# Kernel optimization log

Measured on AMD Instinct MI355X. Metric: run time of the kernel, lower is better.

Reference implementation:

```python
import jax, jax.numpy as jnp
import numpy as np

N_NODES = 50000
N_EDGES = 800000
N_GRAPHS = 256
F_IN = 128
H = 64
N_CLASSES = 10


def setup_inputs() -> dict:
    key = jax.random.key(0)
    ks = jax.random.split(key, 12)
    x = jax.random.normal(ks[0], (N_NODES, F_IN), dtype=jnp.float32)
    edge_index = jax.random.randint(ks[1], (2, N_EDGES), 0, N_NODES, dtype=jnp.int64)
    batch = jnp.sort(jax.random.randint(ks[2], (N_NODES,), 0, N_GRAPHS, dtype=jnp.int64))
    def glorot(k, fan_in, fan_out):
        lim = np.sqrt(6.0 / (fan_in + fan_out)).astype(np.float32)
        return jax.random.uniform(k, (fan_in, fan_out), jnp.float32, -lim, lim)
    return {
        "x": x,
        "edge_index": edge_index,
        "batch": batch,
        "W1": glorot(ks[3], F_IN, H), "b1": jnp.zeros((H,), jnp.float32),
        "W2": glorot(ks[4], H, H),    "b2": jnp.zeros((H,), jnp.float32),
        "W3": glorot(ks[5], H, H),    "b3": jnp.zeros((H,), jnp.float32),
        "Wm": glorot(ks[6], H, N_CLASSES), "bm": jnp.zeros((N_CLASSES,), jnp.float32),
    }


def _gcn_norm(edge_index, n_nodes):
    # Add self-loops, unit edge weights, symmetric normalization (PyG gcn_norm).
    loops = jnp.arange(n_nodes, dtype=edge_index.dtype)
    row = jnp.concatenate([edge_index[0], loops])  # source
    col = jnp.concatenate([edge_index[1], loops])  # target (aggregation index)
    deg = jax.ops.segment_sum(jnp.ones_like(col, dtype=jnp.float32), col,
                              num_segments=n_nodes)
    dinv = jnp.where(deg > 0, jax.lax.rsqrt(deg), 0.0)
    norm = dinv[row] * dinv[col]  # [E + N]
    return row, col, norm


def _gcn_conv(x, row, col, norm, W, b, n_nodes):
    h = x @ W                                   # [N, H] dense transform
    msg = h[row] * norm[:, None]                # gather + scale  [E+N, H]
    out = jax.ops.segment_sum(msg, col, num_segments=n_nodes)  # scatter-add
    return out + b


def _l2_normalize(x, eps=1e-12):
    n = jnp.sqrt(jnp.sum(x * x, axis=-1, keepdims=True))
    return x / jnp.maximum(n, eps)


def reference(x, edge_index, batch, W1, b1, W2, b2, W3, b3, Wm, bm):
    n = x.shape[0]
    row, col, norm = _gcn_norm(edge_index, n)
    h = x
    for (W, b) in ((W1, b1), (W2, b2), (W3, b3)):
        h = _gcn_conv(h, row, col, norm, W, b, n)
        h = _l2_normalize(h)       # emb_normalize
        h = jax.nn.relu(h)         # gnn_non_linear
    node_emb = h
    # global_mean_pool over graphs
    sums = jax.ops.segment_sum(h, batch, num_segments=N_GRAPHS)
    counts = jax.ops.segment_sum(jnp.ones((n,), jnp.float32), batch,
                                 num_segments=N_GRAPHS)
    graph_emb = sums / jnp.maximum(counts, 1.0)[:, None]
    logits = graph_emb @ Wm + bm
    probs = jax.nn.softmax(logits, axis=-1)
    return logits, probs, node_emb, graph_emb
```

## Files before the change

### kernel.cpp

```cpp
#include <hip/hip_runtime.h>
#include <math.h>

#define HH 64
#define BSH 8
#define BSZ 256
#define HBLK 256
#define HSTRIDE (HBLK * 256)

typedef _Float16 half_t;
typedef _Float16 half4_t __attribute__((ext_vector_type(4)));

__global__ __launch_bounds__(256, 3)
void k_gemm1_hist(const float* __restrict__ x, const float* __restrict__ W,
                  half_t* __restrict__ out, int n,
                  const int* __restrict__ col, int E, int* __restrict__ ph) {
    constexpr int FIN = 128;
    constexpr int KC = 32;
    __shared__ __align__(16) float Ws[FIN][HH];
    __shared__ __align__(16) float xs_t[KC][68];
    __shared__ int hh[BSZ];
    const int tid = threadIdx.x;
    const int bid = blockIdx.x;

    if (bid < HBLK) {
        hh[tid] = 0;
        __syncthreads();
        for (int e = bid * 256 + tid; e < E; e += HSTRIDE)
            atomicAdd(&hh[col[e] >> BSH], 1);
        __syncthreads();
        ph[bid * BSZ + tid] = hh[tid];
    }

    const int tx = tid & 15;
    const int ty = tid >> 4;
    const int node0 = bid * 64;
    if (node0 >= n) return;

    for (int i = tid * 4; i < FIN * HH; i += 1024)
        *(float4*)&Ws[0][i] = *(const float4*)&W[i];

    float acc[4][4] = {};
    const int rr0 = tid >> 3;
    const int cc  = (tid & 7) * 4;

    for (int kc = 0; kc < FIN; kc += KC) {
        __syncthreads();
        for (int rr = rr0; rr < 64; rr += 32) {
            float4 v = make_float4(0.f, 0.f, 0.f, 0.f);
            if (node0 + rr < n) v = *(const float4*)&x[(size_t)(node0 + rr) * FIN + kc + cc];
            xs_t[cc + 0][rr] = v.x;
            xs_t[cc + 1][rr] = v.y;
            xs_t[cc + 2][rr] = v.z;
            xs_t[cc + 3][rr] = v.w;
        }
        __syncthreads();
#pragma unroll 4
        for (int k = 0; k < KC; ++k) {
            float4 a4 = *(const float4*)&xs_t[k][ty * 4];
            float4 b4 = *(const float4*)&Ws[kc + k][tx * 4];
            acc[0][0] = fmaf(a4.x, b4.x, acc[0][0]);
            acc[0][1] = fmaf(a4.x, b4.y, acc[0][1]);
            acc[0][2] = fmaf(a4.x, b4.z, acc[0][2]);
            acc[0][3] = fmaf(a4.x, b4.w, acc[0][3]);
            acc[1][0] = fmaf(a4.y, b4.x, acc[1][0]);
            acc[1][1] = fmaf(a4.y, b4.y, acc[1][1]);
            acc[1][2] = fmaf(a4.y, b4.z, acc[1][2]);
            acc[1][3] = fmaf(a4.y, b4.w, acc[1][3]);
            acc[2][0] = fmaf(a4.z, b4.x, acc[2][0]);
            acc[2][1] = fmaf(a4.z, b4.y, acc[2][1]);
            acc[2][2] = fmaf(a4.z, b4.z, acc[2][2]);
            acc[2][3] = fmaf(a4.z, b4.w, acc[2][3]);
            acc[3][0] = fmaf(a4.w, b4.x, acc[3][0]);
            acc[3][1] = fmaf(a4.w, b4.y, acc[3][1]);
            acc[3][2] = fmaf(a4.w, b4.z, acc[3][2]);
            acc[3][3] = fmaf(a4.w, b4.w, acc[3][3]);
        }
    }
#pragma unroll
    for (int i = 0; i < 4; ++i) {
        int node = node0 + ty * 4 + i;
        if (node < n) {
            half4_t o = {(half_t)acc[i][0], (half_t)acc[i][1],
                         (half_t)acc[i][2], (half_t)acc[i][3]};
            *(half4_t*)(out + (size_t)node * HH + tx * 4) = o;
        }
    }
}

__global__ __launch_bounds__(256) void k_bscatter2(const int* __restrict__ row,
                                                   const int* __restrict__ col, int E,
                                                   const int* __restrict__ ph,
                                                   int* __restrict__ base,
                                                   int* __restrict__ pair, int nb) {
    __shared__ int cur[BSZ];
    __shared__ int ssc[BSZ];
    const int b = blockIdx.x;
    const int t = threadIdx.x;
    int before = 0, total = 0;
    for (int k = 0; k < HBLK; ++k) {
        int v = ph[k * BSZ + t];
        total += v;
        if (k < b) before += v;
    }
    ssc[t] = total;
    __syncthreads();
    for (int d = 1; d < 256; d <<= 1) {
        int x2 = ssc[t];
        if (t >= d) x2 += ssc[t - d];
        __syncthreads();
        ssc[t] = x2;
        __syncthreads();
    }
    int excl = ssc[t] - total;
    cur[t] = excl + before;
    if (b == 0) {
        if (t < nb) base[t] = excl;
        if (t == 0) base[nb] = E;
    }
    __syncthreads();
    for (int e = b * 256 + t; e < E; e += HSTRIDE) {
        int c = col[e];
        int pos = atomicAdd(&cur[c >> BSH], 1);
        pair[pos] = (row[e] & 0xFFFF) | ((c & (BSZ - 1)) << 16);
    }
}

__global__ __launch_bounds__(256) void k_bcsr(const int* __restrict__ pair,
                                              const int* __restrict__ base,
                                              int* __restrict__ rowptr,
                                              int* __restrict__ cnt,
                                              float* __restrict__ dinv,
                                              int* __restrict__ csr, int n) {
    __shared__ int lcnt[BSZ];
    __shared__ int ssc[BSZ];
    __shared__ int lcur[BSZ];
    const int b = blockIdx.x;
    const int t = threadIdx.x;
    const int nd0 = b << BSH;
    const int e0 = base[b];
    const int e1 = base[b + 1];

    lcnt[t] = 0;
    __syncthreads();
    for (int e = e0 + t; e < e1; e += 256)
        atomicAdd(&lcnt[(pair[e] >> 16) & (BSZ - 1)], 1);
    __syncthreads();
    int v = lcnt[t];
    ssc[t] = v;
    __syncthreads();
    for (int d = 1; d < 256; d <<= 1) {
        int x2 = ssc[t];
        if (t >= d) x2 += ssc[t - d];
        __syncthreads();
        ssc[t] = x2;
        __syncthreads();
    }
    int excl = ssc[t] - v;
    lcur[t] = e0 + excl;
    int node = nd0 + t;
    if (node < n) {
        rowptr[node] = e0 + excl;
        cnt[node]    = v;
        dinv[node]   = rsqrtf((float)(v + 1));
    }
    __syncthreads();
    for (int e = e0 + t; e < e1; e += 256) {
        int pr = pair[e];
        int pos = atomicAdd(&lcur[(pr >> 16) & (BSZ - 1)], 1);
        csr[pos] = pr & 0xFFFF;
    }
}

template<int FIN>
__global__ __launch_bounds__(256, 4)
void k_gemm(const half_t* __restrict__ xin, const float* __restrict__ W,
            const float* __restrict__ dinv, half_t* __restrict__ out, int n) {
    constexpr int KC = 32;
    __shared__ __align__(16) float Ws[FIN][HH];
    __shared__ __align__(16) float xs_t[KC][68];
    const int tid = threadIdx.x;
    const int tx = tid & 15;
    const int ty = tid >> 4;
    const int node0 = blockIdx.x * 64;
    if (node0 >= n) return;

    for (int i = tid * 4; i < FIN * HH; i += 1024)
        *(float4*)&Ws[0][i] = *(const float4*)&W[i];

    float acc[4][4] = {};
    const int rr0 = tid >> 3;
    const int cc  = (tid & 7) * 4;

    for (int kc = 0; kc < FIN; kc += KC) {
        __syncthreads();
        for (int rr = rr0; rr < 64; rr += 32) {
            float4 v = make_float4(0.f, 0.f, 0.f, 0.f);
            if (node0 + rr < n) {
                half4_t hv = *(const half4_t*)(xin + (size_t)(node0 + rr) * FIN + kc + cc);
                v = make_float4((float)hv.x, (float)hv.y, (float)hv.z, (float)hv.w);
            }
            xs_t[cc + 0][rr] = v.x;
            xs_t[cc + 1][rr] = v.y;
            xs_t[cc + 2][rr] = v.z;
            xs_t[cc + 3][rr] = v.w;
        }
        __syncthreads();
#pragma unroll 4
        for (int k = 0; k < KC; ++k) {
            float4 a4 = *(const float4*)&xs_t[k][ty * 4];
            float4 b4 = *(const float4*)&Ws[kc + k][tx * 4];
            acc[0][0] = fmaf(a4.x, b4.x, acc[0][0]);
            acc[0][1] = fmaf(a4.x, b4.y, acc[0][1]);
            acc[0][2] = fmaf(a4.x, b4.z, acc[0][2]);
            acc[0][3] = fmaf(a4.x, b4.w, acc[0][3]);
            acc[1][0] = fmaf(a4.y, b4.x, acc[1][0]);
            acc[1][1] = fmaf(a4.y, b4.y, acc[1][1]);
            acc[1][2] = fmaf(a4.y, b4.z, acc[1][2]);
            acc[1][3] = fmaf(a4.y, b4.w, acc[1][3]);
            acc[2][0] = fmaf(a4.z, b4.x, acc[2][0]);
            acc[2][1] = fmaf(a4.z, b4.y, acc[2][1]);
            acc[2][2] = fmaf(a4.z, b4.z, acc[2][2]);
            acc[2][3] = fmaf(a4.z, b4.w, acc[2][3]);
            acc[3][0] = fmaf(a4.w, b4.x, acc[3][0]);
            acc[3][1] = fmaf(a4.w, b4.y, acc[3][1]);
            acc[3][2] = fmaf(a4.w, b4.z, acc[3][2]);
            acc[3][3] = fmaf(a4.w, b4.w, acc[3][3]);
        }
    }
#pragma unroll
    for (int i = 0; i < 4; ++i) {
        int node = node0 + ty * 4 + i;
        if (node < n) {
            float d = dinv[node];
            half4_t o = {(half_t)(acc[i][0] * d), (half_t)(acc[i][1] * d),
                         (half_t)(acc[i][2] * d), (half_t)(acc[i][3] * d)};
            *(half4_t*)(out + (size_t)node * HH + tx * 4) = o;
        }
    }
}

template<bool WEIGHTED, bool HOUT>
__global__ __launch_bounds__(256) void k_gather_q(const half_t* __restrict__ lin,
                                                  const int* __restrict__ csr,
                                                  const int* __restrict__ rowptr,
                                                  const int* __restrict__ cnt,
                                                  const float* __restrict__ dinv,
                                                  const float* __restrict__ b,
                                                  void* __restrict__ hout, int n) {
    int node = blockIdx.x * 4 + (threadIdx.x >> 6);
    int lane = threadIdx.x & 63;
    if (node >= n) return;
    const int q  = lane >> 4;
    const int fl = (lane & 15) * 4;
    int start = rowptr[node];
    int end = start + cnt[node];
    float di = dinv[node];

    float4 a0 = make_float4(0.f, 0.f, 0.f, 0.f);
    float4 a1 = make_float4(0.f, 0.f, 0.f, 0.f);

    for (int base = start; base < end; base += 64) {
        int m = end - base; if (m > 64) m = 64;
        int idx = base + lane;
        int   sv = (idx < end) ? csr[idx] : 0;
        float wv;
        if (WEIGHTED) wv = (idx < end) ? dinv[sv] : 0.f;
        else          wv = (idx < end) ? 1.f : 0.f;
        for (int j = 0; j < m; j += 16) {
            int l = j + q * 4;
            int   s0 = __shfl(sv, l, 64);
            int   s1 = __shfl(sv, l + 1, 64);
            int   s2 = __shfl(sv, l + 2, 64);
            int   s3 = __shfl(sv, l + 3, 64);
            float w0 = __shfl(wv, l, 64);
            float w1 = __shfl(wv, l + 1, 64);
            float w2 = __shfl(wv, l + 2, 64);
            float w3 = __shfl(wv, l + 3, 64);
            half4_t v0 = *(const half4_t*)&lin[(size_t)s0 * HH + fl];
            half4_t v1 = *(const half4_t*)&lin[(size_t)s1 * HH + fl];
            half4_t v2 = *(const half4_t*)&lin[(size_t)s2 * HH + fl];
            half4_t v3 = *(const half4_t*)&lin[(size_t)s3 * HH + fl];
            a0.x = fmaf(w0, (float)v0.x, a0.x); a0.y = fmaf(w0, (float)v0.y, a0.y);
            a0.z = fmaf(w0, (float)v0.z, a0.z); a0.w = fmaf(w0, (float)v0.w, a0.w);
            a1.x = fmaf(w1, (float)v1.x, a1.x); a1.y = fmaf(w1, (float)v1.y, a1.y);
            a1.z = fmaf(w1, (float)v1.z, a1.z); a1.w = fmaf(w1, (float)v1.w, a1.w);
            a0.x = fmaf(w2, (float)v2.x, a0.x); a0.y = fmaf(w2, (float)v2.y, a0.y);
            a0.z = fmaf(w2, (float)v2.z, a0.z); a0.w = fmaf(w2, (float)v2.w, a0.w);
            a1.x = fmaf(w3, (float)v3.x, a1.x); a1.y = fmaf(w3, (float)v3.y, a1.y);
            a1.z = fmaf(w3, (float)v3.z, a1.z); a1.w = fmaf(w3, (float)v3.w, a1.w);
        }
    }
    float4 acc = make_float4(a0.x + a1.x, a0.y + a1.y, a0.z + a1.z, a0.w + a1.w);
#pragma unroll
    for (int off = 16; off < 64; off <<= 1) {
        acc.x += __shfl_xor(acc.x, off, 64);
        acc.y += __shfl_xor(acc.y, off, 64);
        acc.z += __shfl_xor(acc.z, off, 64);
        acc.w += __shfl_xor(acc.w, off, 64);
    }
    half4_t self = *(const half4_t*)&lin[(size_t)node * HH + fl];
    float sw = WEIGHTED ? di : 1.f;
    acc.x = fmaf(sw, (float)self.x, acc.x);
    acc.y = fmaf(sw, (float)self.y, acc.y);
    acc.z = fmaf(sw, (float)self.z, acc.z);
    acc.w = fmaf(sw, (float)self.w, acc.w);
    float4 b4 = *(const float4*)&b[fl];
    float4 v4 = make_float4(fmaf(di, acc.x, b4.x), fmaf(di, acc.y, b4.y),
                            fmaf(di, acc.z, b4.z), fmaf(di, acc.w, b4.w));
    float ss = v4.x * v4.x + v4.y * v4.y + v4.z * v4.z + v4.w * v4.w;
#pragma unroll
    for (int off = 1; off < 16; off <<= 1) ss += __shfl_xor(ss, off, 64);
    float inv = 1.f / fmaxf(sqrtf(ss), 1e-12f);
    v4.x = fmaxf(v4.x * inv, 0.f);
    v4.y = fmaxf(v4.y * inv, 0.f);
    v4.z = fmaxf(v4.z * inv, 0.f);
    v4.w = fmaxf(v4.w * inv, 0.f);
    if (q == 0) {
        if constexpr (HOUT) {
            half4_t o = {(half_t)v4.x, (half_t)v4.y, (half_t)v4.z, (half_t)v4.w};
            *(half4_t*)((half_t*)hout + (size_t)node * HH + fl) = o;
        } else {
            *(float4*)((float*)hout + (size_t)node * HH + fl) = v4;
        }
    }
}

__global__ __launch_bounds__(256) void k_poolfinal(const float* __restrict__ node_emb,
                                                   const int* __restrict__ batch,
                                                   const float* __restrict__ Wm,
                                                   const float* __restrict__ bm,
                                                   float* __restrict__ logits,
                                                   float* __restrict__ probs,
                                                   float* __restrict__ graph_emb, int n) {
    __shared__ float part[4][HH];
    __shared__ float semb[HH];
    __shared__ float slog[16];
    const int g = blockIdx.x;
    const int tid = threadIdx.x;
    const int lane = tid & 63, w = tid >> 6;

    int lo = 0, hi = n;
    while (lo < hi) { int mid = (lo + hi) >> 1; if (batch[mid] < g) lo = mid + 1; else hi = mid; }
    const int s = lo;
    hi = n;
    while (lo < hi) { int mid = (lo + hi) >> 1; if (batch[mid] < g + 1) lo = mid + 1; else hi = mid; }
    const int e2 = lo;

    float acc = 0.f;
    for (int i = s + w; i < e2; i += 4) acc += node_emb[(size_t)i * HH + lane];
    part[w][lane] = acc;
    __syncthreads();
    if (tid < HH) {
        float m = part[0][tid] + part[1][tid] + part[2][tid] + part[3][tid];
        m /= fmaxf((float)(e2 - s), 1.f);
        graph_emb[(size_t)g * HH + tid] = m;
        semb[tid] = m;
    }
    __syncthreads();
    if (tid < 10) {
        float a2 = bm[tid];
        for (int k = 0; k < HH; ++k) a2 = fmaf(semb[k], Wm[k * 10 + tid], a2);
        slog[tid] = a2;
    }
    __syncthreads();
    if (tid < 10) {
        float mx = -1e30f;
        for (int j = 0; j < 10; ++j) mx = fmaxf(mx, slog[j]);
        float den = 0.f;
        for (int j = 0; j < 10; ++j) den += __expf(slog[j] - mx);
        float lg = slog[tid];
        logits[g * 10 + tid] = lg;
        probs[g * 10 + tid] = __expf(lg - mx) / den;
    }
}


extern "C" void kernel_launch(void* const* d_in, const int* in_sizes, int n_in,
                              void* d_out, int out_size, void* d_ws, size_t ws_size,
                              hipStream_t stream) {
    const float* x     = (const float*)d_in[0];
    const int*   ei    = (const int*)  d_in[1];
    const int*   batch = (const int*)  d_in[2];
    const float* W1 = (const float*)d_in[3];  const float* b1 = (const float*)d_in[4];
    const float* W2 = (const float*)d_in[5];  const float* b2 = (const float*)d_in[6];
    const float* W3 = (const float*)d_in[7];  const float* b3 = (const float*)d_in[8];
    const float* Wm = (const float*)d_in[9];  const float* bm = (const float*)d_in[10];

    const int N = in_sizes[2];
    const int E = in_sizes[1] / 2;
    const int G = (out_size - N * HH) / (2 * 10 + HH);
    const int NB = (N + BSZ - 1) >> BSH;

    const int* row = ei;
    const int* col = ei + E;

    float* out       = (float*)d_out;
    float* logits    = out;
    float* probs     = out + (size_t)G * 10;
    float* node_emb  = out + (size_t)2 * G * 10;
    float* graph_emb = node_emb + (size_t)N * HH;

    char* w = (char*)d_ws;
    auto alloc = [&](size_t bytes) { char* p = w; w += (bytes + 255) & ~(size_t)255; return p; };
    float* dinv    = (float*)alloc((size_t)N * 4);
    int*   cnt     = (int*)  alloc((size_t)N * 4);
    int*   rowptr  = (int*)  alloc((size_t)N * 4);
    int*   ph      = (int*)  alloc((size_t)HBLK * BSZ * 4);
    int*   base    = (int*)  alloc((size_t)(NB + 1) * 4);
    int*   pairbuf = (int*)  alloc((size_t)E * 4);
    int*   csr     = (int*)  alloc((size_t)E * 4);
    half_t* bufA   = (half_t*)alloc((size_t)N * HH * 2);
    half_t* bufB   = (half_t*)alloc((size_t)N * HH * 2);

    const int B = 256;
    dim3 blk(B);
    int node_blocks = (N + 3) / 4;
    int gemm_blocks = (N + 63) / 64;
    int g1_blocks = gemm_blocks > HBLK ? gemm_blocks : HBLK;

    k_gemm1_hist<<<g1_blocks, blk, 0, stream>>>(x, W1, bufA, N, col, E, ph);
    k_bscatter2<<<HBLK, blk, 0, stream>>>(row, col, E, ph, base, pairbuf, NB);
    k_bcsr<<<NB, blk, 0, stream>>>(pairbuf, base, rowptr, cnt, dinv, csr, N);

    k_gather_q<true, true><<<node_blocks, blk, 0, stream>>>(bufA, csr, rowptr, cnt, dinv, b1, bufB, N);
    k_gemm<64><<<gemm_blocks, blk, 0, stream>>>(bufB, W2, dinv, bufA, N);
    k_gather_q<false, true><<<node_blocks, blk, 0, stream>>>(bufA, csr, rowptr, cnt, dinv, b2, bufB, N);
    k_gemm<64><<<gemm_blocks, blk, 0, stream>>>(bufB, W3, dinv, bufA, N);
    k_gather_q<false, false><<<node_blocks, blk, 0, stream>>>(bufA, csr, rowptr, cnt, dinv, b3, node_emb, N);

    k_poolfinal<<<G, blk, 0, stream>>>(node_emb, batch, Wm, bm, logits, probs, graph_emb, N);
}
```

Measured before the change: 269.9 us.

## Split features into two half-planes and defer L2 normalisation to consumers

Node feature buffers are split into two 32-wide fp16 planes. Each gather kernel launches twice as many blocks, one per plane, so the randomly gathered working set per pass is halved and should sit better in cache. The gather now writes unnormalised pre-activation values plus per-plane sums of squares; the following GEMM and the pooling kernel apply the L2 normalisation and ReLU while loading. This adds per-row norm reads and doubles the index and CSR traffic in the gather, and the pool kernel now also writes node_emb.

```diff
diff --git a/kernel.cpp b/kernel.cpp
--- a/kernel.cpp
+++ b/kernel.cpp
@@ -2,17 +2,19 @@
 #include <math.h>
 
 #define HH 64
+#define HF 32
 #define BSH 8
 #define BSZ 256
 #define HBLK 256
 #define HSTRIDE (HBLK * 256)
 
 typedef _Float16 half_t;
+typedef _Float16 half2_t __attribute__((ext_vector_type(2)));
 typedef _Float16 half4_t __attribute__((ext_vector_type(4)));
 
 __global__ __launch_bounds__(256, 3)
 void k_gemm1_hist(const float* __restrict__ x, const float* __restrict__ W,
-                  half_t* __restrict__ out, int n,
+                  half_t* __restrict__ lo, half_t* __restrict__ hi, int n,
                   const int* __restrict__ col, int E, int* __restrict__ ph) {
     constexpr int FIN = 128;
     constexpr int KC = 32;
@@ -82,7 +84,8 @@
         if (node < n) {
             half4_t o = {(half_t)acc[i][0], (half_t)acc[i][1],
                          (half_t)acc[i][2], (half_t)acc[i][3]};
-            *(half4_t*)(out + (size_t)node * HH + tx * 4) = o;
+            if (tx < 8) *(half4_t*)&lo[(size_t)node * HF + tx * 4]        = o;
+            else        *(half4_t*)&hi[(size_t)node * HF + tx * 4 - 32]   = o;
         }
     }
 }
@@ -173,8 +176,10 @@
 
 template<int FIN>
 __global__ __launch_bounds__(256, 4)
-void k_gemm(const half_t* __restrict__ xin, const float* __restrict__ W,
-            const float* __restrict__ dinv, half_t* __restrict__ out, int n) {
+void k_gemm(const half_t* __restrict__ xlo, const half_t* __restrict__ xhi,
+            const float* __restrict__ ssLo, const float* __restrict__ ssHi,
+            const float* __restrict__ W, const float* __restrict__ dinv,
+            half_t* __restrict__ olo, half_t* __restrict__ ohi, int n) {
     constexpr int KC = 32;
     __shared__ __align__(16) float Ws[FIN][HH];
     __shared__ __align__(16) float xs_t[KC][68];
@@ -194,10 +199,17 @@
     for (int kc = 0; kc < FIN; kc += KC) {
         __syncthreads();
         for (int rr = rr0; rr < 64; rr += 32) {
+            int r = node0 + rr;
             float4 v = make_float4(0.f, 0.f, 0.f, 0.f);
-            if (node0 + rr < n) {
-                half4_t hv = *(const half4_t*)(xin + (size_t)(node0 + rr) * FIN + kc + cc);
-                v = make_float4((float)hv.x, (float)hv.y, (float)hv.z, (float)hv.w);
+            if (r < n) {
+                float invr = 1.f / fmaxf(sqrtf(ssLo[r] + ssHi[r]), 1e-12f);
+                int f = kc + cc;
+                const half_t* src = (f < 32) ? xlo : xhi;
+                half4_t hv = *(const half4_t*)&src[(size_t)r * HF + (f & 31)];
+                v = make_float4(invr * fmaxf((float)hv.x, 0.f),
+                                invr * fmaxf((float)hv.y, 0.f),
+                                invr * fmaxf((float)hv.z, 0.f),
+                                invr * fmaxf((float)hv.w, 0.f));
             }
             xs_t[cc + 0][rr] = v.x;
             xs_t[cc + 1][rr] = v.y;
@@ -234,30 +246,41 @@
             float d = dinv[node];
             half4_t o = {(half_t)(acc[i][0] * d), (half_t)(acc[i][1] * d),
                          (half_t)(acc[i][2] * d), (half_t)(acc[i][3] * d)};
-            *(half4_t*)(out + (size_t)node * HH + tx * 4) = o;
-        }
-    }
-}
-
-template<bool WEIGHTED, bool HOUT>
-__global__ __launch_bounds__(256) void k_gather_q(const half_t* __restrict__ lin,
+            if (tx < 8) *(half4_t*)&olo[(size_t)node * HF + tx * 4]      = o;
+            else        *(half4_t*)&ohi[(size_t)node * HF + tx * 4 - 32] = o;
+        }
+    }
+}
+
+template<bool WEIGHTED>
+__global__ __launch_bounds__(256) void k_gather_s(const half_t* __restrict__ lin_lo,
+                                                  const half_t* __restrict__ lin_hi,
                                                   const int* __restrict__ csr,
                                                   const int* __restrict__ rowptr,
                                                   const int* __restrict__ cnt,
                                                   const float* __restrict__ dinv,
                                                   const float* __restrict__ b,
-                                                  void* __restrict__ hout, int n) {
-    int node = blockIdx.x * 4 + (threadIdx.x >> 6);
-    int lane = threadIdx.x & 63;
+                                                  half_t* __restrict__ h_lo,
+                                                  half_t* __restrict__ h_hi,
+                                                  float* __restrict__ ssLo,
+                                                  float* __restrict__ ssHi, int n) {
+    const int pass = blockIdx.x & 1;
+    const int grp  = blockIdx.x >> 1;
+    const int lane = threadIdx.x & 63;
+    const int node = grp * 4 + (threadIdx.x >> 6);
     if (node >= n) return;
-    const int q  = lane >> 4;
-    const int fl = (lane & 15) * 4;
+    const half_t* __restrict__ lin = pass ? lin_hi : lin_lo;
+    half_t* __restrict__ ho  = pass ? h_hi : h_lo;
+    float*  __restrict__ ssp = pass ? ssHi : ssLo;
+
+    const int q   = lane >> 4;
+    const int fl2 = (lane & 15) * 2;
+    const int bf  = pass * HF + fl2;
     int start = rowptr[node];
     int end = start + cnt[node];
     float di = dinv[node];
 
-    float4 a0 = make_float4(0.f, 0.f, 0.f, 0.f);
-    float4 a1 = make_float4(0.f, 0.f, 0.f, 0.f);
+    float ax0 = 0.f, ay0 = 0.f, ax1 = 0.f, ay1 = 0.f;
 
     for (int base = start; base < end; base += 64) {
         int m = end - base; if (m > 64) m = 64;
@@ -276,61 +299,47 @@
             float w1 = __shfl(wv, l + 1, 64);
             float w2 = __shfl(wv, l + 2, 64);
             float w3 = __shfl(wv, l + 3, 64);
-            half4_t v0 = *(const half4_t*)&lin[(size_t)s0 * HH + fl];
-            half4_t v1 = *(const half4_t*)&lin[(size_t)s1 * HH + fl];
-            half4_t v2 = *(const half4_t*)&lin[(size_t)s2 * HH + fl];
-            half4_t v3 = *(const half4_t*)&lin[(size_t)s3 * HH + fl];
-            a0.x = fmaf(w0, (float)v0.x, a0.x); a0.y = fmaf(w0, (float)v0.y, a0.y);
-            a0.z = fmaf(w0, (float)v0.z, a0.z); a0.w = fmaf(w0, (float)v0.w, a0.w);
-            a1.x = fmaf(w1, (float)v1.x, a1.x); a1.y = fmaf(w1, (float)v1.y, a1.y);
-            a1.z = fmaf(w1, (float)v1.z, a1.z); a1.w = fmaf(w1, (float)v1.w, a1.w);
-            a0.x = fmaf(w2, (float)v2.x, a0.x); a0.y = fmaf(w2, (float)v2.y, a0.y);
-            a0.z = fmaf(w2, (float)v2.z, a0.z); a0.w = fmaf(w2, (float)v2.w, a0.w);
-            a1.x = fmaf(w3, (float)v3.x, a1.x); a1.y = fmaf(w3, (float)v3.y, a1.y);
-            a1.z = fmaf(w3, (float)v3.z, a1.z); a1.w = fmaf(w3, (float)v3.w, a1.w);
-        }
-    }
-    float4 acc = make_float4(a0.x + a1.x, a0.y + a1.y, a0.z + a1.z, a0.w + a1.w);
-#pragma unroll
-    for (int off = 16; off < 64; off <<= 1) {
-        acc.x += __shfl_xor(acc.x, off, 64);
-        acc.y += __shfl_xor(acc.y, off, 64);
-        acc.z += __shfl_xor(acc.z, off, 64);
-        acc.w += __shfl_xor(acc.w, off, 64);
-    }
-    half4_t self = *(const half4_t*)&lin[(size_t)node * HH + fl];
+            half2_t v0 = *(const half2_t*)&lin[(size_t)s0 * HF + fl2];
+            half2_t v1 = *(const half2_t*)&lin[(size_t)s1 * HF + fl2];
+            half2_t v2 = *(const half2_t*)&lin[(size_t)s2 * HF + fl2];
+            half2_t v3 = *(const half2_t*)&lin[(size_t)s3 * HF + fl2];
+            ax0 = fmaf(w0, (float)v0.x, ax0); ay0 = fmaf(w0, (float)v0.y, ay0);
+            ax1 = fmaf(w1, (float)v1.x, ax1); ay1 = fmaf(w1, (float)v1.y, ay1);
+            ax0 = fmaf(w2, (float)v2.x, ax0); ay0 = fmaf(w2, (float)v2.y, ay0);
+            ax1 = fmaf(w3, (float)v3.x, ax1); ay1 = fmaf(w3, (float)v3.y, ay1);
+        }
+    }
+    float ax = ax0 + ax1, ay = ay0 + ay1;
+    ax += __shfl_xor(ax, 16, 64); ay += __shfl_xor(ay, 16, 64);
+    ax += __shfl_xor(ax, 32, 64); ay += __shfl_xor(ay, 32, 64);
+    half2_t self = *(const half2_t*)&lin[(size_t)node * HF + fl2];
     float sw = WEIGHTED ? di : 1.f;
-    acc.x = fmaf(sw, (float)self.x, acc.x);
-    acc.y = fmaf(sw, (float)self.y, acc.y);
-    acc.z = fmaf(sw, (float)self.z, acc.z);
-    acc.w = fmaf(sw, (float)self.w, acc.w);
-    float4 b4 = *(const float4*)&b[fl];
-    float4 v4 = make_float4(fmaf(di, acc.x, b4.x), fmaf(di, acc.y, b4.y),
-                            fmaf(di, acc.z, b4.z), fmaf(di, acc.w, b4.w));
-    float ss = v4.x * v4.x + v4.y * v4.y + v4.z * v4.z + v4.w * v4.w;
-#pragma unroll
-    for (int off = 1; off < 16; off <<= 1) ss += __shfl_xor(ss, off, 64);
-    float inv = 1.f / fmaxf(sqrtf(ss), 1e-12f);
-    v4.x = fmaxf(v4.x * inv, 0.f);
-    v4.y = fmaxf(v4.y * inv, 0.f);
-    v4.z = fmaxf(v4.z * inv, 0.f);
-    v4.w = fmaxf(v4.w * inv, 0.f);
+    ax = fmaf(sw, (float)self.x, ax);
+    ay = fmaf(sw, (float)self.y, ay);
+    float vx = fmaf(di, ax, b[bf]);
+    float vy = fmaf(di, ay, b[bf + 1]);
+    float ss = vx * vx + vy * vy;
+    ss += __shfl_xor(ss, 1, 64);
+    ss += __shfl_xor(ss, 2, 64);
+    ss += __shfl_xor(ss, 4, 64);
+    ss += __shfl_xor(ss, 8, 64);
     if (q == 0) {
-        if constexpr (HOUT) {
-            half4_t o = {(half_t)v4.x, (half_t)v4.y, (half_t)v4.z, (half_t)v4.w};
-            *(half4_t*)((half_t*)hout + (size_t)node * HH + fl) = o;
-        } else {
-            *(float4*)((float*)hout + (size_t)node * HH + fl) = v4;
-        }
-    }
-}
-
-__global__ __launch_bounds__(256) void k_poolfinal(const float* __restrict__ node_emb,
+        half2_t o = {(half_t)vx, (half_t)vy};
+        *(half2_t*)&ho[(size_t)node * HF + fl2] = o;
+        if (lane == 0) ssp[node] = ss;
+    }
+}
+
+__global__ __launch_bounds__(256) void k_poolfinal(const half_t* __restrict__ h_lo,
+                                                   const half_t* __restrict__ h_hi,
+                                                   const float* __restrict__ ssLo,
+                                                   const float* __restrict__ ssHi,
                                                    const int* __restrict__ batch,
                                                    const float* __restrict__ Wm,
                                                    const float* __restrict__ bm,
                                                    float* __restrict__ logits,
                                                    float* __restrict__ probs,
+                                                   float* __restrict__ node_emb,
                                                    float* __restrict__ graph_emb, int n) {
     __shared__ float part[4][HH];
     __shared__ float semb[HH];
@@ -347,7 +356,14 @@
     const int e2 = lo;
 
     float acc = 0.f;
-    for (int i = s + w; i < e2; i += 4) acc += node_emb[(size_t)i * HH + lane];
+    for (int i = s + w; i < e2; i += 4) {
+        float invr = 1.f / fmaxf(sqrtf(ssLo[i] + ssHi[i]), 1e-12f);
+        half_t hv = (lane < HF) ? h_lo[(size_t)i * HF + lane]
+                                : h_hi[(size_t)i * HF + lane - HF];
+        float emb = invr * fmaxf((float)hv, 0.f);
+        node_emb[(size_t)i * HH + lane] = emb;
+        acc += emb;
+    }
     part[w][lane] = acc;
     __syncthreads();
     if (tid < HH) {
@@ -409,24 +425,33 @@
     int*   base    = (int*)  alloc((size_t)(NB + 1) * 4);
     int*   pairbuf = (int*)  alloc((size_t)E * 4);
     int*   csr     = (int*)  alloc((size_t)E * 4);
-    half_t* bufA   = (half_t*)alloc((size_t)N * HH * 2);
-    half_t* bufB   = (half_t*)alloc((size_t)N * HH * 2);
+    half_t* A_lo   = (half_t*)alloc((size_t)N * HF * 2);
+    half_t* A_hi   = (half_t*)alloc((size_t)N * HF * 2);
+    half_t* B_lo   = (half_t*)alloc((size_t)N * HF * 2);
+    half_t* B_hi   = (half_t*)alloc((size_t)N * HF * 2);
+    float* ssLo    = (float*)alloc((size_t)N * 4);
+    float* ssHi    = (float*)alloc((size_t)N * 4);
 
     const int B = 256;
     dim3 blk(B);
     int node_blocks = (N + 3) / 4;
+    int gather_blocks = 2 * node_blocks;
     int gemm_blocks = (N + 63) / 64;
     int g1_blocks = gemm_blocks > HBLK ? gemm_blocks : HBLK;
 
-    k_gemm1_hist<<<g1_blocks, blk, 0, stream>>>(x, W1, bufA, N, col, E, ph);
+    k_gemm1_hist<<<g1_blocks, blk, 0, stream>>>(x, W1, A_lo, A_hi, N, col, E, ph);
     k_bscatter2<<<HBLK, blk, 0, stream>>>(row, col, E, ph, base, pairbuf, NB);
     k_bcsr<<<NB, blk, 0, stream>>>(pairbuf, base, rowptr, cnt, dinv, csr, N);
 
-    k_gather_q<true, true><<<node_blocks, blk, 0, stream>>>(bufA, csr, rowptr, cnt, dinv, b1, bufB, N);
-    k_gemm<64><<<gemm_blocks, blk, 0, stream>>>(bufB, W2, dinv, bufA, N);
-    k_gather_q<false, true><<<node_blocks, blk, 0, stream>>>(bufA, csr, rowptr, cnt, dinv, b2, bufB, N);
-    k_gemm<64><<<gemm_blocks, blk, 0, stream>>>(bufB, W3, dinv, bufA, N);
-    k_gather_q<false, false><<<node_blocks, blk, 0, stream>>>(bufA, csr, rowptr, cnt, dinv, b3, node_emb, N);
-
-    k_poolfinal<<<G, blk, 0, stream>>>(node_emb, batch, Wm, bm, logits, probs, graph_emb, N);
-}
+    k_gather_s<true><<<gather_blocks, blk, 0, stream>>>(A_lo, A_hi, csr, rowptr, cnt,
+                                                        dinv, b1, B_lo, B_hi, ssLo, ssHi, N);
+    k_gemm<64><<<gemm_blocks, blk, 0, stream>>>(B_lo, B_hi, ssLo, ssHi, W2, dinv, A_lo, A_hi, N);
+    k_gather_s<false><<<gather_blocks, blk, 0, stream>>>(A_lo, A_hi, csr, rowptr, cnt,
+                                                         dinv, b2, B_lo, B_hi, ssLo, ssHi, N);
+    k_gemm<64><<<gemm_blocks, blk, 0, stream>>>(B_lo, B_hi, ssLo, ssHi, W3, dinv, A_lo, A_hi, N);
+    k_gather_s<false><<<gather_blocks, blk, 0, stream>>>(A_lo, A_hi, csr, rowptr, cnt,
+                                                         dinv, b3, B_lo, B_hi, ssLo, ssHi, N);
+
+    k_poolfinal<<<G, blk, 0, stream>>>(B_lo, B_hi, ssLo, ssHi, batch, Wm, bm,
+                                       logits, probs, node_emb, graph_emb, N);
+}
```

Result: slower. 316.5 us (+17.2%).
